# Optimization experiments

Measured on AMD Instinct MI355X. Metric: run time of the kernel, lower is better.

The kernel has to match this reference:

```python
import jax, jax.numpy as jnp
import numpy as np

MUL = 128            # multiplicity of 0e and 1o node irreps
N_NODES = 10000
N_EDGES = 160000
R_BASIS = 8          # edge_feats_irreps.num_irreps
HIDDEN = 64
W_NUMEL = 4 * MUL    # conv_tp.weight_numel (4 uvu paths, edge mul = 1)
SQRT3 = 3.0 ** 0.5
SILU_2MOM = 1.679177   # e3nn normalize2mom constant for SiLU
AVG_NUM_NEIGHBORS = 10.0


def setup_inputs() -> dict:
    key = jax.random.key(0)
    ks = jax.random.split(key, 12)
    rn = lambda k, s: jax.random.normal(k, s, dtype=jnp.float32)
    return {
        "node_feats": rn(ks[0], (N_NODES, 4 * MUL)),        # 128x0e + 128x1o
        "edge_attrs": rn(ks[1], (N_EDGES, 4)),               # 1x0e + 1x1o spherical harmonics
        "edge_feats": rn(ks[2], (N_EDGES, R_BASIS)),         # 8x0e radial basis
        "edge_index": jax.random.randint(ks[3], (2, N_EDGES), 0, N_NODES),
        "W_up0": rn(ks[4], (MUL, MUL)),                      # linear_up, 0e block
        "W_up1": rn(ks[5], (MUL, MUL)),                      # linear_up, 1o block
        "W_mlp1": rn(ks[6], (R_BASIS, HIDDEN)),
        "W_mlp2": rn(ks[7], (HIDDEN, HIDDEN)),
        "W_mlp3": rn(ks[8], (HIDDEN, HIDDEN)),
        "W_mlp4": rn(ks[9], (HIDDEN, W_NUMEL)),
        "W_out0": rn(ks[10], (2 * MUL, MUL)),                # linear: 256x0e -> 128x0e
        "W_out1": rn(ks[11], (2 * MUL, MUL)),                # linear: 256x1o -> 128x1o
    }


def _lin_irreps(x0, x1, W0, W1):
    # equivariant o3.Linear: per-irrep channel mixing with 1/sqrt(fan_in)
    y0 = (x0 @ W0) / jnp.sqrt(jnp.float32(W0.shape[0]))
    y1 = jnp.einsum('num,uv->nvm', x1, W1) / jnp.sqrt(jnp.float32(W1.shape[0]))
    return y0, y1


def _forward(node_feats, edge_attrs, edge_feats, edge_index,
             W_up0, W_up1, W_mlp1, W_mlp2, W_mlp3, W_mlp4, W_out0, W_out1):
    num_nodes = node_feats.shape[0]
    sender, receiver = edge_index[0], edge_index[1]

    # split node feats into irrep blocks: [N,128] scalars, [N,128,3] vectors
    x0 = node_feats[:, :MUL]
    x1 = node_feats[:, MUL:].reshape(num_nodes, MUL, 3)
    x0, x1 = _lin_irreps(x0, x1, W_up0, W_up1)  # linear_up

    # radial MLP (e3nn FullyConnectedNet with normalized SiLU) -> per-edge TP weights
    h = edge_feats
    for W in (W_mlp1, W_mlp2, W_mlp3):
        h = SILU_2MOM * jax.nn.silu((h @ W) / jnp.sqrt(jnp.float32(W.shape[0])))
    tpw = (h @ W_mlp4) / jnp.sqrt(jnp.float32(W_mlp4.shape[0]))  # [E, 4*MUL]
    w1, w2, w3, w4 = jnp.split(tpw, 4, axis=-1)  # per-path [E, MUL]

    # gather sender features
    s0 = x0[sender]              # [E, MUL]
    s1 = x1[sender]              # [E, MUL, 3]
    y0 = edge_attrs[:, 0:1]      # [E, 1]  (0e sh)
    y1 = edge_attrs[:, 1:4]      # [E, 3]  (1o sh)

    # weighted uvu CG tensor product (component norm: alpha = sqrt(2l_out+1), w3j sum-sq = 1)
    p1 = w1 * s0 * y0                                    # 0e x 0e -> 0e  [E, MUL]
    p2 = (w2 * s0)[:, :, None] * y1[:, None, :]          # 0e x 1o -> 1o  [E, MUL, 3]
    p3 = w3[:, :, None] * s1 * y0[:, None, :]            # 1o x 0e -> 1o  [E, MUL, 3]
    p4 = w4 * jnp.einsum('eum,em->eu', s1, y1) / SQRT3   # 1o x 1o -> 0e  [E, MUL]

    # irreps_mid.simplify() = 256x0e + 256x1o
    m0 = jnp.concatenate([p1, p4], axis=-1)              # [E, 2*MUL]
    m1 = jnp.concatenate([p2, p3], axis=1)               # [E, 2*MUL, 3]

    # scatter-sum over receivers
    msg0 = jax.ops.segment_sum(m0, receiver, num_segments=num_nodes)
    msg1 = jax.ops.segment_sum(m1, receiver, num_segments=num_nodes)

    o0, o1 = _lin_irreps(msg0, msg1, W_out0, W_out1)
    out = jnp.concatenate([o0, o1.reshape(num_nodes, 3 * MUL)], axis=-1)
    return out / AVG_NUM_NEIGHBORS


def reference(node_feats, edge_attrs, edge_feats, edge_index,
              W_up0, W_up1, W_mlp1, W_mlp2, W_mlp3, W_mlp4, W_out0, W_out1):
    return _forward(node_feats, edge_attrs, edge_feats, edge_index,
                    W_up0, W_up1, W_mlp1, W_mlp2, W_mlp3, W_mlp4, W_out0, W_out1)
```

## Files before the change

### kernel.cpp

```cpp
#include <hip/hip_runtime.h>
#include <stdint.h>

#define NN 10000
#define NE 160000

typedef short short8 __attribute__((ext_vector_type(8)));
typedef float f32x4 __attribute__((ext_vector_type(4)));

__device__ __forceinline__ float bf2f(unsigned short u) {
    return __uint_as_float(((uint32_t)u) << 16);
}
__device__ __forceinline__ float bflo(uint32_t u) { return __uint_as_float(u << 16); }
__device__ __forceinline__ float bfhi(uint32_t u) { return __uint_as_float(u & 0xffff0000u); }
__device__ __forceinline__ unsigned short f2bf(float f) {
    uint32_t u = __float_as_uint(f);
    u += 0x7fffu + ((u >> 16) & 1u);
    return (unsigned short)(u >> 16);
}
__device__ __forceinline__ uint32_t pack2(float lo, float hi) {
    return (uint32_t)f2bf(lo) | ((uint32_t)f2bf(hi) << 16);
}
__device__ __forceinline__ float silu2(float x) {
    return 1.679177f * x / (1.f + __expf(-x));
}

__global__ __launch_bounds__(256) void k_wup(const float* __restrict__ Wu0,
                                             const float* __restrict__ Wu1,
                                             unsigned short* __restrict__ w0T,
                                             unsigned short* __restrict__ w1T) {
    const float s = 0.08838834764831845f;
    for (int i = threadIdx.x + blockIdx.x * 256; i < 16384; i += 256 * 64) {
        int u = i >> 7, v = i & 127;
        w0T[v * 128 + u] = f2bf(Wu0[i] * s);
        w1T[v * 128 + u] = f2bf(Wu1[i] * s);
    }
}

__global__ __launch_bounds__(256) void k_prep(const float* __restrict__ nf,
                                              unsigned short* __restrict__ x0b,
                                              unsigned short* __restrict__ x1b) {
    int idx = blockIdx.x * 256 + threadIdx.x;
    int n = idx >> 7, u = idx & 127;
    const float* row = nf + (size_t)n * 512;
    x0b[(size_t)n * 128 + u] = f2bf(row[u]);
    const float* p = row + 128 + u * 3;
    x1b[(size_t)n * 128 + u]                = f2bf(p[0]);
    x1b[1280000 + (size_t)n * 128 + u]      = f2bf(p[1]);
    x1b[2560000 + (size_t)n * 128 + u]      = f2bf(p[2]);
}

__global__ __launch_bounds__(256) void k_upg(const unsigned short* __restrict__ x0b,
                                             const unsigned short* __restrict__ x1b,
                                             const unsigned short* __restrict__ w0T,
                                             const unsigned short* __restrict__ w1T,
                                             float* __restrict__ xw) {
    int wave = threadIdx.x >> 6, lane = threadIdx.x & 63;
    int wid = blockIdx.x * 4 + wave;
    if (wid >= 1250) return;
    int tile = wid >> 1, half = wid & 1;
    int n0 = tile * 16;
    int lm = lane & 15, lq = lane >> 4;

    uint4 A0[4], A1[3][4];
    const unsigned short* a0r = x0b + (size_t)(n0 + lm) * 128 + lq * 8;
#pragma unroll
    for (int kf = 0; kf < 4; ++kf) A0[kf] = *(const uint4*)(a0r + kf * 32);
#pragma unroll
    for (int m = 0; m < 3; ++m) {
        const unsigned short* a1r = x1b + 1280000 * (size_t)m + (size_t)(n0 + lm) * 128 + lq * 8;
#pragma unroll
        for (int kf = 0; kf < 4; ++kf) A1[m][kf] = *(const uint4*)(a1r + kf * 32);
    }

    for (int vq = 0; vq < 4; ++vq) {
        int vt = half * 4 + vq;
        const unsigned short* b0r = w0T + (vt * 16 + lm) * 128 + lq * 8;
        const unsigned short* b1r = w1T + (vt * 16 + lm) * 128 + lq * 8;
        f32x4 acc0 = {0.f, 0.f, 0.f, 0.f};
#pragma unroll
        for (int kf = 0; kf < 4; ++kf) {
            short8 b = __builtin_bit_cast(short8, *(const uint4*)(b0r + kf * 32));
            acc0 = __builtin_amdgcn_mfma_f32_16x16x32_bf16(
                __builtin_bit_cast(short8, A0[kf]), b, acc0, 0, 0, 0);
        }
        f32x4 acc1[3];
#pragma unroll
        for (int m = 0; m < 3; ++m) acc1[m] = (f32x4){0.f, 0.f, 0.f, 0.f};
#pragma unroll
        for (int kf = 0; kf < 4; ++kf) {
            short8 b = __builtin_bit_cast(short8, *(const uint4*)(b1r + kf * 32));
#pragma unroll
            for (int m = 0; m < 3; ++m)
                acc1[m] = __builtin_amdgcn_mfma_f32_16x16x32_bf16(
                    __builtin_bit_cast(short8, A1[m][kf]), b, acc1[m], 0, 0, 0);
        }
        int col = vt * 16 + lm;
#pragma unroll
        for (int r = 0; r < 4; ++r) {
            float* o = xw + (size_t)(n0 + lq * 4 + r) * 512;
            o[col] = acc0[r];
            o[128 + col] = acc1[0][r];
            o[256 + col] = acc1[1][r];
            o[384 + col] = acc1[2][r];
        }
    }
}

__global__ __launch_bounds__(256) void k_wmlp(const float* __restrict__ W1,
                                              const float* __restrict__ W2,
                                              const float* __restrict__ W3,
                                              unsigned short* __restrict__ w1Tp,
                                              unsigned short* __restrict__ w2T,
                                              unsigned short* __restrict__ w3T) {
    int t = threadIdx.x;
    for (int i = t; i < 2048; i += 256) {
        int jj = i >> 5, k = i & 31;
        w1Tp[i] = (k < 8) ? f2bf(W1[k * 64 + jj] * 0.3535533905932738f) : 0;
    }
    for (int i = t; i < 4096; i += 256) {
        int jj = i >> 6, k = i & 63;
        w2T[i] = f2bf(W2[k * 64 + jj] * 0.125f);
        w3T[i] = f2bf(W3[k * 64 + jj] * 0.125f);
    }
}

__global__ __launch_bounds__(256) void k_mlp(const float* __restrict__ ef,
                                             const unsigned short* __restrict__ w1Tp,
                                             const unsigned short* __restrict__ w2T,
                                             const unsigned short* __restrict__ w3T,
                                             unsigned short* __restrict__ h3w) {
    __shared__ __align__(16) unsigned short hs_all[4][16 * 72];
    int wave = threadIdx.x >> 6, lane = threadIdx.x & 63;
    int lm = lane & 15, lq = lane >> 4;
    int e0 = blockIdx.x * 64 + wave * 16;
    unsigned short* h = hs_all[wave];
    unsigned short* hrow = h + lm * 72;

    uint4 A1[4];
#pragma unroll
    for (int mt = 0; mt < 4; ++mt)
        A1[mt] = *(const uint4*)(w1Tp + (mt * 16 + lm) * 32 + lq * 8);
    uint4 b = {0, 0, 0, 0};
    if (lq == 0) {
        const float4* p = (const float4*)(ef + (size_t)(e0 + lm) * 8);
        float4 x = p[0], y = p[1];
        b.x = pack2(x.x, x.y); b.y = pack2(x.z, x.w);
        b.z = pack2(y.x, y.y); b.w = pack2(y.z, y.w);
    }
    short8 bb = __builtin_bit_cast(short8, b);
#pragma unroll
    for (int mt = 0; mt < 4; ++mt) {
        f32x4 acc = {0.f, 0.f, 0.f, 0.f};
        acc = __builtin_amdgcn_mfma_f32_16x16x32_bf16(
            __builtin_bit_cast(short8, A1[mt]), bb, acc, 0, 0, 0);
        uint2 v;
        v.x = pack2(silu2(acc[0]), silu2(acc[1]));
        v.y = pack2(silu2(acc[2]), silu2(acc[3]));
        *(uint2*)(hrow + mt * 16 + lq * 4) = v;
    }

    uint4 A2[4][2];
#pragma unroll
    for (int mt = 0; mt < 4; ++mt)
#pragma unroll
        for (int kf = 0; kf < 2; ++kf)
            A2[mt][kf] = *(const uint4*)(w2T + (mt * 16 + lm) * 64 + kf * 32 + lq * 8);
    {
        short8 B0 = __builtin_bit_cast(short8, *(const uint4*)(hrow + lq * 8));
        short8 B1 = __builtin_bit_cast(short8, *(const uint4*)(hrow + 32 + lq * 8));
#pragma unroll
        for (int mt = 0; mt < 4; ++mt) {
            f32x4 acc = {0.f, 0.f, 0.f, 0.f};
            acc = __builtin_amdgcn_mfma_f32_16x16x32_bf16(
                __builtin_bit_cast(short8, A2[mt][0]), B0, acc, 0, 0, 0);
            acc = __builtin_amdgcn_mfma_f32_16x16x32_bf16(
                __builtin_bit_cast(short8, A2[mt][1]), B1, acc, 0, 0, 0);
            uint2 v;
            v.x = pack2(silu2(acc[0]), silu2(acc[1]));
            v.y = pack2(silu2(acc[2]), silu2(acc[3]));
            *(uint2*)(hrow + mt * 16 + lq * 4) = v;
        }
    }

    uint4 A3[4][2];
#pragma unroll
    for (int mt = 0; mt < 4; ++mt)
#pragma unroll
        for (int kf = 0; kf < 2; ++kf)
            A3[mt][kf] = *(const uint4*)(w3T + (mt * 16 + lm) * 64 + kf * 32 + lq * 8);
    {
        short8 B0 = __builtin_bit_cast(short8, *(const uint4*)(hrow + lq * 8));
        short8 B1 = __builtin_bit_cast(short8, *(const uint4*)(hrow + 32 + lq * 8));
#pragma unroll
        for (int mt = 0; mt < 4; ++mt) {
            f32x4 acc = {0.f, 0.f, 0.f, 0.f};
            acc = __builtin_amdgcn_mfma_f32_16x16x32_bf16(
                __builtin_bit_cast(short8, A3[mt][0]), B0, acc, 0, 0, 0);
            acc = __builtin_amdgcn_mfma_f32_16x16x32_bf16(
                __builtin_bit_cast(short8, A3[mt][1]), B1, acc, 0, 0, 0);
            uint2 v;
            v.x = pack2(silu2(acc[0]), silu2(acc[1]));
            v.y = pack2(silu2(acc[2]), silu2(acc[3]));
            *(uint2*)(hrow + mt * 16 + lq * 4) = v;
        }
    }

#pragma unroll
    for (int q = 0; q < 2; ++q) {
        int c = lane + q * 64;
        int row = c >> 3, col = (c & 7) * 8;
        *(uint4*)(h3w + (size_t)(e0 + row) * 64 + col) =
            *(const uint4*)(h + row * 72 + col);
    }
}

__global__ void k_zero(int* __restrict__ p, int n) {
    int i = blockIdx.x * 256 + threadIdx.x;
    if (i < n) p[i] = 0;
}
__global__ void k_hist(const int* __restrict__ ei, int* __restrict__ counts) {
    int e = blockIdx.x * 256 + threadIdx.x;
    if (e < NE) atomicAdd(&counts[ei[NE + e]], 1);
}
__global__ __launch_bounds__(1024) void k_scan(const int* __restrict__ counts,
                                               int* __restrict__ offs,
                                               int* __restrict__ cursor) {
    __shared__ int sums[1024];
    int t = threadIdx.x;
    int base = t * 10;
    int s = 0;
    for (int i = 0; i < 10; ++i) {
        int idx = base + i;
        if (idx < NN) s += counts[idx];
    }
    sums[t] = s;
    __syncthreads();
    for (int d = 1; d < 1024; d <<= 1) {
        int v = (t >= d) ? sums[t - d] : 0;
        __syncthreads();
        if (t >= d) sums[t] += v;
        __syncthreads();
    }
    int run = (t == 0) ? 0 : sums[t - 1];
    for (int i = 0; i < 10; ++i) {
        int idx = base + i;
        if (idx < NN) {
            offs[idx] = run;
            cursor[idx] = run;
            run += counts[idx];
        }
    }
    if (t == 0) offs[NN] = NE;
}
__global__ void k_fill(const int* __restrict__ ei, int* __restrict__ cursor,
                       int* __restrict__ elist) {
    int e = blockIdx.x * 256 + threadIdx.x;
    if (e < NE) {
        int slot = atomicAdd(&cursor[ei[NE + e]], 1);
        elist[slot] = e;
    }
}
__global__ void k_gather(const int* __restrict__ ei, const float* __restrict__ ea,
                         const int* __restrict__ elist,
                         int* __restrict__ eis, float4* __restrict__ eap) {
    int i = blockIdx.x * 256 + threadIdx.x;
    if (i < NE) {
        int e = elist[i];
        eis[i] = ei[e];
        eap[i] = *(const float4*)(ea + (size_t)e * 4);
    }
}

__global__ void k_w4t(const float* __restrict__ W4, unsigned short* __restrict__ w4T) {
    int idx = blockIdx.x * 256 + threadIdx.x;
    int k = idx >> 9, c = idx & 511;
    w4T[c * 64 + k] = f2bf(W4[idx]);
}
__global__ void k_wt2(const float* __restrict__ Wo0, const float* __restrict__ Wo1,
                      unsigned short* __restrict__ woT0, unsigned short* __restrict__ woT1) {
    int idx = blockIdx.x * 256 + threadIdx.x;
    int u = idx >> 7, v = idx & 127;
    woT0[v * 256 + u] = f2bf(Wo0[idx]);
    woT1[v * 256 + u] = f2bf(Wo1[idx]);
}

__global__ __launch_bounds__(64, 4) void k_msg2(const float* __restrict__ xw,
                                                const unsigned short* __restrict__ h3w,
                                                const unsigned short* __restrict__ w4T,
                                                const int* __restrict__ eis,
                                                const float4* __restrict__ eap,
                                                const int* __restrict__ offs,
                                                const int* __restrict__ elist,
                                                unsigned short* __restrict__ msgb) {
    __shared__ __align__(8) unsigned short wl[16][130];
    int bid = blockIdx.x;
    int n = bid >> 2, j = bid & 3;
    int lw = threadIdx.x;
    int lm = lw & 15, lq = lw >> 4;
    int c0 = lw * 2;
    int beg = offs[n], end = offs[n + 1];
    float a0 = 0.f, a1 = 0.f, a2 = 0.f, a3 = 0.f, a4 = 0.f, a5 = 0.f;

    if (end > beg) {
        const int last = end - 1;
        const unsigned short* aw = w4T + (size_t)(j * 128 + lm) * 64 + lq * 8;

        for (int cbeg = beg; cbeg < end; cbeg += 16) {
            int slot = cbeg + lm;
            slot = slot <= last ? slot : last;
            int esrc = elist[slot];
            const unsigned short* hr = h3w + (size_t)esrc * 64 + lq * 8;
            short8 B0 = __builtin_bit_cast(short8, *(const uint4*)(hr));
            short8 B1 = __builtin_bit_cast(short8, *(const uint4*)(hr + 32));
#pragma unroll
            for (int mt = 0; mt < 8; ++mt) {
                uint4 a0r = *(const uint4*)(aw + mt * 1024);
                uint4 a1r = *(const uint4*)(aw + mt * 1024 + 32);
                f32x4 acc = {0.f, 0.f, 0.f, 0.f};
                acc = __builtin_amdgcn_mfma_f32_16x16x32_bf16(
                    __builtin_bit_cast(short8, a0r), B0, acc, 0, 0, 0);
                acc = __builtin_amdgcn_mfma_f32_16x16x32_bf16(
                    __builtin_bit_cast(short8, a1r), B1, acc, 0, 0, 0);
                uint2 v;
                v.x = pack2(acc[0] * 0.125f, acc[1] * 0.125f);
                v.y = pack2(acc[2] * 0.125f, acc[3] * 0.125f);
                *(uint2*)&wl[lm][mt * 16 + lq * 4] = v;
            }

            int cend = cbeg + 16 < end ? cbeg + 16 : end;
            if (j == 0) {
                for (int g = cbeg; g < cend; g += 8) {
                    int s_[8]; float wa[8], wb[8], ey[8]; float2 x[8];
#pragma unroll
                    for (int k = 0; k < 8; ++k) {
                        int idx = g + k;
                        int cl = idx <= last ? idx : last;
                        s_[k] = eis[cl];
                    }
#pragma unroll
                    for (int k = 0; k < 8; ++k) {
                        int idx = g + k;
                        int cl = idx <= last ? idx : last;
                        int e = idx - cbeg;
                        uint32_t w = *(const uint32_t*)&wl[e][c0];
                        wa[k] = idx <= last ? bflo(w) : 0.f;
                        wb[k] = idx <= last ? bfhi(w) : 0.f;
                        ey[k] = eap[cl].x;
                        x[k] = *(const float2*)(xw + (size_t)s_[k] * 512 + c0);
                    }
#pragma unroll
                    for (int k = 0; k < 8; ++k) {
                        a0 += wa[k] * x[k].x * ey[k];
                        a1 += wb[k] * x[k].y * ey[k];
                    }
                }
            } else if (j == 1) {
                for (int g = cbeg; g < cend; g += 8) {
                    int s_[8]; float wa[8], wb[8], ex[8], ey[8], ez[8]; float2 x[8];
#pragma unroll
                    for (int k = 0; k < 8; ++k) {
                        int idx = g + k;
                        int cl = idx <= last ? idx : last;
                        s_[k] = eis[cl];
                    }
#pragma unroll
                    for (int k = 0; k < 8; ++k) {
                        int idx = g + k;
                        int cl = idx <= last ? idx : last;
                        int e = idx - cbeg;
                        uint32_t w = *(const uint32_t*)&wl[e][c0];
                        wa[k] = idx <= last ? bflo(w) : 0.f;
                        wb[k] = idx <= last ? bfhi(w) : 0.f;
                        float4 ev = eap[cl];
                        ex[k] = ev.y; ey[k] = ev.z; ez[k] = ev.w;
                        x[k] = *(const float2*)(xw + (size_t)s_[k] * 512 + c0);
                    }
#pragma unroll
                    for (int k = 0; k < 8; ++k) {
                        float ta = wa[k] * x[k].x, tb = wb[k] * x[k].y;
                        a0 += ta * ex[k]; a1 += ta * ey[k]; a2 += ta * ez[k];
                        a3 += tb * ex[k]; a4 += tb * ey[k]; a5 += tb * ez[k];
                    }
                }
            } else if (j == 2) {
                for (int g = cbeg; g < cend; g += 8) {
                    int s_[8]; float wa[8], wb[8], ey[8];
                    float2 x0[8], x1[8], x2[8];
#pragma unroll
                    for (int k = 0; k < 8; ++k) {
                        int idx = g + k;
                        int cl = idx <= last ? idx : last;
                        s_[k] = eis[cl];
                    }
#pragma unroll
                    for (int k = 0; k < 8; ++k) {
                        int idx = g + k;
                        int cl = idx <= last ? idx : last;
                        int e = idx - cbeg;
                        uint32_t w = *(const uint32_t*)&wl[e][c0];
                        wa[k] = idx <= last ? bflo(w) : 0.f;
                        wb[k] = idx <= last ? bfhi(w) : 0.f;
                        ey[k] = eap[cl].x;
                        const float* xr = xw + (size_t)s_[k] * 512 + c0;
                        x0[k] = *(const float2*)(xr + 128);
                        x1[k] = *(const float2*)(xr + 256);
                        x2[k] = *(const float2*)(xr + 384);
                    }
#pragma unroll
                    for (int k = 0; k < 8; ++k) {
                        float f0 = wa[k] * ey[k], f1 = wb[k] * ey[k];
                        a0 += f0 * x0[k].x; a1 += f0 * x1[k].x; a2 += f0 * x2[k].x;
                        a3 += f1 * x0[k].y; a4 += f1 * x1[k].y; a5 += f1 * x2[k].y;
                    }
                }
            } else {
                for (int g = cbeg; g < cend; g += 8) {
                    int s_[8]; float wa[8], wb[8], ex[8], ey[8], ez[8];
                    float2 x0[8], x1[8], x2[8];
#pragma unroll
                    for (int k = 0; k < 8; ++k) {
                        int idx = g + k;
                        int cl = idx <= last ? idx : last;
                        s_[k] = eis[cl];
                    }
#pragma unroll
                    for (int k = 0; k < 8; ++k) {
                        int idx = g + k;
                        int cl = idx <= last ? idx : last;
                        int e = idx - cbeg;
                        uint32_t w = *(const uint32_t*)&wl[e][c0];
                        wa[k] = idx <= last ? bflo(w) : 0.f;
                        wb[k] = idx <= last ? bfhi(w) : 0.f;
                        float4 ev = eap[cl];
                        ex[k] = ev.y; ey[k] = ev.z; ez[k] = ev.w;
                        const float* xr = xw + (size_t)s_[k] * 512 + c0;
                        x0[k] = *(const float2*)(xr + 128);
                        x1[k] = *(const float2*)(xr + 256);
                        x2[k] = *(const float2*)(xr + 384);
                    }
#pragma unroll
                    for (int k = 0; k < 8; ++k) {
                        float dta = x0[k].x * ex[k] + x1[k].x * ey[k] + x2[k].x * ez[k];
                        float dtb = x0[k].y * ex[k] + x1[k].y * ey[k] + x2[k].y * ez[k];
                        a0 += wa[k] * dta * 0.5773502691896258f;
                        a1 += wb[k] * dtb * 0.5773502691896258f;
                    }
                }
            }
        }
    }

    unsigned short* mr = msgb + (size_t)n * 1024;
    if (j == 0) {
        *(uint32_t*)(mr + c0) = pack2(a0, a1);
    } else if (j == 1) {
        *(uint32_t*)(mr + 256 + c0)       = pack2(a0, a3);
        *(uint32_t*)(mr + 256 + 256 + c0) = pack2(a1, a4);
        *(uint32_t*)(mr + 256 + 512 + c0) = pack2(a2, a5);
    } else if (j == 2) {
        *(uint32_t*)(mr + 256 + 128 + c0)       = pack2(a0, a3);
        *(uint32_t*)(mr + 256 + 256 + 128 + c0) = pack2(a1, a4);
        *(uint32_t*)(mr + 256 + 512 + 128 + c0) = pack2(a2, a5);
    } else {
        *(uint32_t*)(mr + 128 + c0) = pack2(a0, a1);
    }
}

__global__ __launch_bounds__(256) void k_out0(const unsigned short* __restrict__ msgb,
                                              const unsigned short* __restrict__ woT,
                                              float* __restrict__ out) {
    int wave = threadIdx.x >> 6, lane = threadIdx.x & 63;
    int wid = blockIdx.x * 4 + wave;
    if (wid >= NN / 16) return;
    int n0 = wid * 16;
    int lm = lane & 15, lq = lane >> 4;
    uint4 A[8];
    const unsigned short* ar = msgb + (size_t)(n0 + lm) * 1024 + lq * 8;
#pragma unroll
    for (int kf = 0; kf < 8; ++kf) A[kf] = *(const uint4*)(ar + kf * 32);
    const unsigned short* br = woT + lm * 256 + lq * 8;
    float* ob = out + (size_t)n0 * 512;
    for (int vt = 0; vt < 8; ++vt) {
        f32x4 acc = {0.f, 0.f, 0.f, 0.f};
#pragma unroll
        for (int kf = 0; kf < 8; ++kf) {
            uint4 b = *(const uint4*)(br + vt * 16 * 256 + kf * 32);
            acc = __builtin_amdgcn_mfma_f32_16x16x32_bf16(
                __builtin_bit_cast(short8, A[kf]), __builtin_bit_cast(short8, b), acc, 0, 0, 0);
        }
#pragma unroll
        for (int r = 0; r < 4; ++r)
            ob[(size_t)(lq * 4 + r) * 512 + vt * 16 + lm] = acc[r] * 0.00625f;
    }
}

__global__ __launch_bounds__(256) void k_out1(const unsigned short* __restrict__ msgb,
                                              const unsigned short* __restrict__ woT,
                                              float* __restrict__ out) {
    int wave = threadIdx.x >> 6, lane = threadIdx.x & 63;
    int wid = blockIdx.x * 4 + wave;
    if (wid >= NN / 16) return;
    int n0 = wid * 16;
    int lm = lane & 15, lq = lane >> 4;
    uint4 A[3][8];
    const unsigned short* ar = msgb + (size_t)(n0 + lm) * 1024 + 256 + lq * 8;
#pragma unroll
    for (int m = 0; m < 3; ++m)
#pragma unroll
        for (int kf = 0; kf < 8; ++kf)
            A[m][kf] = *(const uint4*)(ar + m * 256 + kf * 32);
    const unsigned short* br = woT + lm * 256 + lq * 8;
    float* ob = out + (size_t)n0 * 512 + 128;
    for (int vt = 0; vt < 8; ++vt) {
        f32x4 acc[3];
#pragma unroll
        for (int m = 0; m < 3; ++m) acc[m] = (f32x4){0.f, 0.f, 0.f, 0.f};
#pragma unroll
        for (int kf = 0; kf < 8; ++kf) {
            uint4 braw = *(const uint4*)(br + vt * 16 * 256 + kf * 32);
            short8 b = __builtin_bit_cast(short8, braw);
#pragma unroll
            for (int m = 0; m < 3; ++m)
                acc[m] = __builtin_amdgcn_mfma_f32_16x16x32_bf16(
                    __builtin_bit_cast(short8, A[m][kf]), b, acc[m], 0, 0, 0);
        }
        int vb = (vt * 16 + lm) * 3;
#pragma unroll
        for (int r = 0; r < 4; ++r) {
            float* o = ob + (size_t)(lq * 4 + r) * 512 + vb;
            o[0] = acc[0][r] * 0.00625f;
            o[1] = acc[1][r] * 0.00625f;
            o[2] = acc[2][r] * 0.00625f;
        }
    }
}

extern "C" void kernel_launch(void* const* d_in, const int* in_sizes, int n_in,
                              void* d_out, int out_size, void* d_ws, size_t ws_size,
                              hipStream_t stream) {
    const float* nf  = (const float*)d_in[0];
    const float* ea  = (const float*)d_in[1];
    const float* ef  = (const float*)d_in[2];
    const int*   ei  = (const int*)d_in[3];
    const float* Wu0 = (const float*)d_in[4];
    const float* Wu1 = (const float*)d_in[5];
    const float* W1  = (const float*)d_in[6];
    const float* W2  = (const float*)d_in[7];
    const float* W3  = (const float*)d_in[8];
    const float* W4  = (const float*)d_in[9];
    const float* Wo0 = (const float*)d_in[10];
    const float* Wo1 = (const float*)d_in[11];
    float* out = (float*)d_out;
    char* ws = (char*)d_ws;

    unsigned short* x0b  = (unsigned short*)ws;
    unsigned short* x1b  = (unsigned short*)(ws + 2560000);
    unsigned short* woT0 = (unsigned short*)ws;
    unsigned short* woT1 = (unsigned short*)(ws + 65536);
    float4*         eap  = (float4*)(ws + 131072);
    int*            eis  = (int*)(ws + 131072 + 2560000);
    float*          xw   = (float*)(ws + 163840000);
    unsigned short* h3w  = (unsigned short*)(ws + 184320000);
    unsigned short* msgb = (unsigned short*)(ws + 204800000);
    unsigned short* w4T  = (unsigned short*)(ws + 225280000);
    int* ib     = (int*)(ws + 225280000 + 65536);
    int* counts = ib;
    int* offs   = ib + 10240;
    int* cursor = ib + 20480;
    int* elist  = ib + 30720;
    unsigned short* w1Tp = (unsigned short*)(ws + 226108416);
    unsigned short* w2T  = (unsigned short*)(ws + 226108416 + 4096);
    unsigned short* w3T  = (unsigned short*)(ws + 226108416 + 12288);
    unsigned short* w0T  = (unsigned short*)(ws + 226128896);
    unsigned short* w1T  = (unsigned short*)(ws + 226161664);

    k_wmlp <<<1, 256, 0, stream>>>(W1, W2, W3, w1Tp, w2T, w3T);
    k_wup  <<<64, 256, 0, stream>>>(Wu0, Wu1, w0T, w1T);
    k_prep <<<5000, 256, 0, stream>>>(nf, x0b, x1b);
    k_upg  <<<313, 256, 0, stream>>>(x0b, x1b, w0T, w1T, xw);
    k_mlp  <<<2500, 256, 0, stream>>>(ef, w1Tp, w2T, w3T, h3w);
    k_w4t  <<<128, 256, 0, stream>>>(W4, w4T);
    k_zero <<<40, 256, 0, stream>>>(counts, NN);
    k_hist <<<625, 256, 0, stream>>>(ei, counts);
    k_scan <<<1, 1024, 0, stream>>>(counts, offs, cursor);
    k_fill <<<625, 256, 0, stream>>>(ei, cursor, elist);
    k_wt2  <<<128, 256, 0, stream>>>(Wo0, Wo1, woT0, woT1);
    k_gather<<<625, 256, 0, stream>>>(ei, ea, elist, eis, eap);
    k_msg2 <<<NN * 4, 64, 0, stream>>>(xw, h3w, w4T, eis, eap, offs, elist, msgb);
    k_out0 <<<157, 256, 0, stream>>>(msgb, woT0, out);
    k_out1 <<<157, 256, 0, stream>>>(msgb, woT1, out);
}
```

Baseline: 429.7 us.

## Merge small prep kernels and restructure message kernel into 256-thread blocks

Folds the weight transposes, count zeroing, histogram and node-feature conversion into two multi-role kernels. It also merges the two output GEMM kernels into one and runs the message kernel with one 256-thread block per node instead of four 64-thread blocks. The goal is fewer kernel launches and less launch and tail overhead. In exchange, the merged output kernel holds more registers per wave, and the merged prep kernels mix workloads within a single grid.

```diff
diff --git a/kernel.cpp b/kernel.cpp
--- a/kernel.cpp
+++ b/kernel.cpp
@@ -24,29 +24,66 @@
     return 1.679177f * x / (1.f + __expf(-x));
 }
 
-__global__ __launch_bounds__(256) void k_wup(const float* __restrict__ Wu0,
+__global__ __launch_bounds__(256) void k_pre(const float* __restrict__ W1,
+                                             const float* __restrict__ W2,
+                                             const float* __restrict__ W3,
+                                             const float* __restrict__ Wu0,
                                              const float* __restrict__ Wu1,
+                                             const float* __restrict__ W4,
+                                             unsigned short* __restrict__ w1Tp,
+                                             unsigned short* __restrict__ w2T,
+                                             unsigned short* __restrict__ w3T,
                                              unsigned short* __restrict__ w0T,
-                                             unsigned short* __restrict__ w1T) {
-    const float s = 0.08838834764831845f;
-    for (int i = threadIdx.x + blockIdx.x * 256; i < 16384; i += 256 * 64) {
-        int u = i >> 7, v = i & 127;
-        w0T[v * 128 + u] = f2bf(Wu0[i] * s);
-        w1T[v * 128 + u] = f2bf(Wu1[i] * s);
-    }
-}
-
-__global__ __launch_bounds__(256) void k_prep(const float* __restrict__ nf,
-                                              unsigned short* __restrict__ x0b,
-                                              unsigned short* __restrict__ x1b) {
-    int idx = blockIdx.x * 256 + threadIdx.x;
-    int n = idx >> 7, u = idx & 127;
-    const float* row = nf + (size_t)n * 512;
-    x0b[(size_t)n * 128 + u] = f2bf(row[u]);
-    const float* p = row + 128 + u * 3;
-    x1b[(size_t)n * 128 + u]                = f2bf(p[0]);
-    x1b[1280000 + (size_t)n * 128 + u]      = f2bf(p[1]);
-    x1b[2560000 + (size_t)n * 128 + u]      = f2bf(p[2]);
+                                             unsigned short* __restrict__ w1T,
+                                             unsigned short* __restrict__ w4T,
+                                             int* __restrict__ counts) {
+    int bid = blockIdx.x, t = threadIdx.x;
+    if (bid == 0) {
+        for (int i = t; i < 2048; i += 256) {
+            int jj = i >> 5, k = i & 31;
+            w1Tp[i] = (k < 8) ? f2bf(W1[k * 64 + jj] * 0.3535533905932738f) : 0;
+        }
+        for (int i = t; i < 4096; i += 256) {
+            int jj = i >> 6, k = i & 63;
+            w2T[i] = f2bf(W2[k * 64 + jj] * 0.125f);
+            w3T[i] = f2bf(W3[k * 64 + jj] * 0.125f);
+        }
+    } else if (bid < 65) {
+        const float s = 0.08838834764831845f;
+        for (int i = t + (bid - 1) * 256; i < 16384; i += 256 * 64) {
+            int u = i >> 7, v = i & 127;
+            w0T[v * 128 + u] = f2bf(Wu0[i] * s);
+            w1T[v * 128 + u] = f2bf(Wu1[i] * s);
+        }
+    } else if (bid < 193) {
+        int idx = (bid - 65) * 256 + t;
+        int k = idx >> 9, c = idx & 511;
+        w4T[c * 64 + k] = f2bf(W4[idx]);
+    } else {
+        int i = (bid - 193) * 256 + t;
+        if (i < NN) counts[i] = 0;
+    }
+}
+
+__global__ __launch_bounds__(256) void k_prep2(const float* __restrict__ nf,
+                                               const int* __restrict__ ei,
+                                               unsigned short* __restrict__ x0b,
+                                               unsigned short* __restrict__ x1b,
+                                               int* __restrict__ counts) {
+    int bid = blockIdx.x;
+    if (bid < 5000) {
+        int idx = bid * 256 + threadIdx.x;
+        int n = idx >> 7, u = idx & 127;
+        const float* row = nf + (size_t)n * 512;
+        x0b[(size_t)n * 128 + u] = f2bf(row[u]);
+        const float* p = row + 128 + u * 3;
+        x1b[(size_t)n * 128 + u]                = f2bf(p[0]);
+        x1b[1280000 + (size_t)n * 128 + u]      = f2bf(p[1]);
+        x1b[2560000 + (size_t)n * 128 + u]      = f2bf(p[2]);
+    } else {
+        int e = (bid - 5000) * 256 + threadIdx.x;
+        if (e < NE) atomicAdd(&counts[ei[NE + e]], 1);
+    }
 }
 
 __global__ __launch_bounds__(256) void k_upg(const unsigned short* __restrict__ x0b,
@@ -106,24 +143,6 @@
     }
 }
 
-__global__ __launch_bounds__(256) void k_wmlp(const float* __restrict__ W1,
-                                              const float* __restrict__ W2,
-                                              const float* __restrict__ W3,
-                                              unsigned short* __restrict__ w1Tp,
-                                              unsigned short* __restrict__ w2T,
-                                              unsigned short* __restrict__ w3T) {
-    int t = threadIdx.x;
-    for (int i = t; i < 2048; i += 256) {
-        int jj = i >> 5, k = i & 31;
-        w1Tp[i] = (k < 8) ? f2bf(W1[k * 64 + jj] * 0.3535533905932738f) : 0;
-    }
-    for (int i = t; i < 4096; i += 256) {
-        int jj = i >> 6, k = i & 63;
-        w2T[i] = f2bf(W2[k * 64 + jj] * 0.125f);
-        w3T[i] = f2bf(W3[k * 64 + jj] * 0.125f);
-    }
-}
-
 __global__ __launch_bounds__(256) void k_mlp(const float* __restrict__ ef,
                                              const unsigned short* __restrict__ w1Tp,
                                              const unsigned short* __restrict__ w2T,
@@ -214,14 +233,6 @@
     }
 }
 
-__global__ void k_zero(int* __restrict__ p, int n) {
-    int i = blockIdx.x * 256 + threadIdx.x;
-    if (i < n) p[i] = 0;
-}
-__global__ void k_hist(const int* __restrict__ ei, int* __restrict__ counts) {
-    int e = blockIdx.x * 256 + threadIdx.x;
-    if (e < NE) atomicAdd(&counts[ei[NE + e]], 1);
-}
 __global__ __launch_bounds__(1024) void k_scan(const int* __restrict__ counts,
                                                int* __restrict__ offs,
                                                int* __restrict__ cursor) {
@@ -271,11 +282,6 @@
     }
 }
 
-__global__ void k_w4t(const float* __restrict__ W4, unsigned short* __restrict__ w4T) {
-    int idx = blockIdx.x * 256 + threadIdx.x;
-    int k = idx >> 9, c = idx & 511;
-    w4T[c * 64 + k] = f2bf(W4[idx]);
-}
 __global__ void k_wt2(const float* __restrict__ Wo0, const float* __restrict__ Wo1,
                       unsigned short* __restrict__ woT0, unsigned short* __restrict__ woT1) {
     int idx = blockIdx.x * 256 + threadIdx.x;
@@ -284,21 +290,21 @@
     woT1[v * 256 + u] = f2bf(Wo1[idx]);
 }
 
-__global__ __launch_bounds__(64, 4) void k_msg2(const float* __restrict__ xw,
-                                                const unsigned short* __restrict__ h3w,
-                                                const unsigned short* __restrict__ w4T,
-                                                const int* __restrict__ eis,
-                                                const float4* __restrict__ eap,
-                                                const int* __restrict__ offs,
-                                                const int* __restrict__ elist,
-                                                unsigned short* __restrict__ msgb) {
-    __shared__ __align__(8) unsigned short wl[16][130];
-    int bid = blockIdx.x;
-    int n = bid >> 2, j = bid & 3;
-    int lw = threadIdx.x;
+__global__ __launch_bounds__(256) void k_msg2(const float* __restrict__ xw,
+                                              const unsigned short* __restrict__ h3w,
+                                              const unsigned short* __restrict__ w4T,
+                                              const int* __restrict__ eis,
+                                              const float4* __restrict__ eap,
+                                              const int* __restrict__ offs,
+                                              const int* __restrict__ elist,
+                                              unsigned short* __restrict__ msgb) {
+    __shared__ __align__(8) unsigned short wl_all[4][16][130];
+    int n = blockIdx.x, t = threadIdx.x;
+    int j = t >> 6, lw = t & 63;
     int lm = lw & 15, lq = lw >> 4;
     int c0 = lw * 2;
     int beg = offs[n], end = offs[n + 1];
+    unsigned short (*wl)[130] = wl_all[j];
     float a0 = 0.f, a1 = 0.f, a2 = 0.f, a3 = 0.f, a4 = 0.f, a5 = 0.f;
 
     if (end > beg) {
@@ -466,71 +472,68 @@
     }
 }
 
-__global__ __launch_bounds__(256) void k_out0(const unsigned short* __restrict__ msgb,
-                                              const unsigned short* __restrict__ woT,
-                                              float* __restrict__ out) {
+__global__ __launch_bounds__(256) void k_out(const unsigned short* __restrict__ msgb,
+                                             const unsigned short* __restrict__ woT0,
+                                             const unsigned short* __restrict__ woT1,
+                                             float* __restrict__ out) {
     int wave = threadIdx.x >> 6, lane = threadIdx.x & 63;
     int wid = blockIdx.x * 4 + wave;
     if (wid >= NN / 16) return;
     int n0 = wid * 16;
     int lm = lane & 15, lq = lane >> 4;
-    uint4 A[8];
     const unsigned short* ar = msgb + (size_t)(n0 + lm) * 1024 + lq * 8;
-#pragma unroll
-    for (int kf = 0; kf < 8; ++kf) A[kf] = *(const uint4*)(ar + kf * 32);
-    const unsigned short* br = woT + lm * 256 + lq * 8;
-    float* ob = out + (size_t)n0 * 512;
-    for (int vt = 0; vt < 8; ++vt) {
-        f32x4 acc = {0.f, 0.f, 0.f, 0.f};
-#pragma unroll
-        for (int kf = 0; kf < 8; ++kf) {
-            uint4 b = *(const uint4*)(br + vt * 16 * 256 + kf * 32);
-            acc = __builtin_amdgcn_mfma_f32_16x16x32_bf16(
-                __builtin_bit_cast(short8, A[kf]), __builtin_bit_cast(short8, b), acc, 0, 0, 0);
-        }
-#pragma unroll
-        for (int r = 0; r < 4; ++r)
-            ob[(size_t)(lq * 4 + r) * 512 + vt * 16 + lm] = acc[r] * 0.00625f;
-    }
-}
-
-__global__ __launch_bounds__(256) void k_out1(const unsigned short* __restrict__ msgb,
-                                              const unsigned short* __restrict__ woT,
-                                              float* __restrict__ out) {
-    int wave = threadIdx.x >> 6, lane = threadIdx.x & 63;
-    int wid = blockIdx.x * 4 + wave;
-    if (wid >= NN / 16) return;
-    int n0 = wid * 16;
-    int lm = lane & 15, lq = lane >> 4;
-    uint4 A[3][8];
-    const unsigned short* ar = msgb + (size_t)(n0 + lm) * 1024 + 256 + lq * 8;
+
+    uint4 A0[8];
+#pragma unroll
+    for (int kf = 0; kf < 8; ++kf) A0[kf] = *(const uint4*)(ar + kf * 32);
+    uint4 A1[3][8];
 #pragma unroll
     for (int m = 0; m < 3; ++m)
 #pragma unroll
         for (int kf = 0; kf < 8; ++kf)
-            A[m][kf] = *(const uint4*)(ar + m * 256 + kf * 32);
-    const unsigned short* br = woT + lm * 256 + lq * 8;
-    float* ob = out + (size_t)n0 * 512 + 128;
-    for (int vt = 0; vt < 8; ++vt) {
-        f32x4 acc[3];
-#pragma unroll
-        for (int m = 0; m < 3; ++m) acc[m] = (f32x4){0.f, 0.f, 0.f, 0.f};
-#pragma unroll
-        for (int kf = 0; kf < 8; ++kf) {
-            uint4 braw = *(const uint4*)(br + vt * 16 * 256 + kf * 32);
-            short8 b = __builtin_bit_cast(short8, braw);
-#pragma unroll
-            for (int m = 0; m < 3; ++m)
-                acc[m] = __builtin_amdgcn_mfma_f32_16x16x32_bf16(
-                    __builtin_bit_cast(short8, A[m][kf]), b, acc[m], 0, 0, 0);
-        }
-        int vb = (vt * 16 + lm) * 3;
-#pragma unroll
-        for (int r = 0; r < 4; ++r) {
-            float* o = ob + (size_t)(lq * 4 + r) * 512 + vb;
-            o[0] = acc[0][r] * 0.00625f;
-            o[1] = acc[1][r] * 0.00625f;
-            o[2] = acc[2][r] * 0.00625f;
+            A1[m][kf] = *(const uint4*)(ar + 256 + m * 256 + kf * 32);
+
+    {
+        const unsigned short* br = woT0 + lm * 256 + lq * 8;
+        float* ob = out + (size_t)n0 * 512;
+        for (int vt = 0; vt < 8; ++vt) {
+            f32x4 acc = {0.f, 0.f, 0.f, 0.f};
+#pragma unroll
+            for (int kf = 0; kf < 8; ++kf) {
+                uint4 b = *(const uint4*)(br + vt * 16 * 256 + kf * 32);
+                acc = __builtin_amdgcn_mfma_f32_16x16x32_bf16(
+                    __builtin_bit_cast(short8, A0[kf]), __builtin_bit_cast(short8, b), acc, 0, 0, 0);
+            }
+#pragma unroll
+            for (int r = 0; r < 4; ++r)
+                ob[(size_t)(lq * 4 + r) * 512 + vt * 16 + lm] = acc[r] * 0.00625f;
+        }
+    }
+
+    {
+        const unsigned short* br = woT1 + lm * 256 + lq * 8;
+        float* ob = out + (size_t)n0 * 512 + 128;
+        for (int vt = 0; vt < 8; ++vt) {
+            f32x4 acc[3];
+#pragma unroll
+            for (int m = 0; m < 3; ++m) acc[m] = (f32x4){0.f, 0.f, 0.f, 0.f};
+#pragma unroll
+            for (int kf = 0; kf < 8; ++kf) {
+                uint4 braw = *(const uint4*)(br + vt * 16 * 256 + kf * 32);
+                short8 b = __builtin_bit_cast(short8, braw);
+#pragma unroll
+                for (int m = 0; m < 3; ++m)
+                    acc[m] = __builtin_amdgcn_mfma_f32_16x16x32_bf16(
+                        __builtin_bit_cast(short8, A1[m][kf]), b, acc[m], 0, 0, 0);
+            }
+            int vb = (vt * 16 + lm) * 3;
+#pragma unroll
+            for (int r = 0; r < 4; ++r) {
+                float* o = ob + (size_t)(lq * 4 + r) * 512 + vb;
+                o[0] = acc[0][r] * 0.00625f;
+                o[1] = acc[1][r] * 0.00625f;
+                o[2] = acc[2][r] * 0.00625f;
+            }
         }
     }
 }
@@ -574,19 +577,15 @@
     unsigned short* w0T  = (unsigned short*)(ws + 226128896);
     unsigned short* w1T  = (unsigned short*)(ws + 226161664);
 
-    k_wmlp <<<1, 256, 0, stream>>>(W1, W2, W3, w1Tp, w2T, w3T);
-    k_wup  <<<64, 256, 0, stream>>>(Wu0, Wu1, w0T, w1T);
-    k_prep <<<5000, 256, 0, stream>>>(nf, x0b, x1b);
-    k_upg  <<<313, 256, 0, stream>>>(x0b, x1b, w0T, w1T, xw);
-    k_mlp  <<<2500, 256, 0, stream>>>(ef, w1Tp, w2T, w3T, h3w);
-    k_w4t  <<<128, 256, 0, stream>>>(W4, w4T);
-    k_zero <<<40, 256, 0, stream>>>(counts, NN);
-    k_hist <<<625, 256, 0, stream>>>(ei, counts);
-    k_scan <<<1, 1024, 0, stream>>>(counts, offs, cursor);
-    k_fill <<<625, 256, 0, stream>>>(ei, cursor, elist);
-    k_wt2  <<<128, 256, 0, stream>>>(Wo0, Wo1, woT0, woT1);
+    k_pre   <<<233, 256, 0, stream>>>(W1, W2, W3, Wu0, Wu1, W4,
+                                      w1Tp, w2T, w3T, w0T, w1T, w4T, counts);
+    k_prep2 <<<5625, 256, 0, stream>>>(nf, ei, x0b, x1b, counts);
+    k_upg   <<<313, 256, 0, stream>>>(x0b, x1b, w0T, w1T, xw);
+    k_mlp   <<<2500, 256, 0, stream>>>(ef, w1Tp, w2T, w3T, h3w);
+    k_scan  <<<1, 1024, 0, stream>>>(counts, offs, cursor);
+    k_fill  <<<625, 256, 0, stream>>>(ei, cursor, elist);
+    k_wt2   <<<128, 256, 0, stream>>>(Wo0, Wo1, woT0, woT1);
     k_gather<<<625, 256, 0, stream>>>(ei, ea, elist, eis, eap);
-    k_msg2 <<<NN * 4, 64, 0, stream>>>(xw, h3w, w4T, eis, eap, offs, elist, msgb);
-    k_out0 <<<157, 256, 0, stream>>>(msgb, woT0, out);
-    k_out1 <<<157, 256, 0, stream>>>(msgb, woT1, out);
-}
+    k_msg2  <<<NN, 256, 0, stream>>>(xw, h3w, w4T, eis, eap, offs, elist, msgb);
+    k_out   <<<157, 256, 0, stream>>>(msgb, woT0, woT1, out);
+}
```

New measurement: 360.8 us. 1.19x faster.
